# Kernel tuning notes

Hardware: AMD Instinct MI355X
Metric: run time of the kernel (lower is better)

## Reference

```python
import jax, jax.numpy as jnp
import numpy as np

N = 10000   # nodes
E = 160000  # edges (avg degree 16)
D_IN = 768
D_HID = 128
HEADS = 4
NEG_SLOPE = 0.2  # PyG GATConv default leaky_relu slope


def setup_inputs() -> dict:
    key = jax.random.key(0)
    ks = jax.random.split(key, 20)
    nrm = lambda k, s, sc: jax.random.normal(k, s, dtype=jnp.float32) * sc
    return {
        "x": nrm(ks[0], (N, D_IN), 1.0),
        "edge_index": jax.random.randint(ks[1], (2, E), 0, N, dtype=jnp.int32),
        "g": nrm(ks[2], (N, D_IN), 1.0),
        # project: Linear(768,128)
        "proj_W": nrm(ks[3], (D_IN, D_HID), D_IN ** -0.5),
        "proj_b": nrm(ks[4], (D_HID,), 0.01),
        # gat1: GATConv(128,128,heads=4), concat -> 512
        "gat1_W": nrm(ks[5], (D_HID, HEADS * D_HID), D_HID ** -0.5),
        "gat1_att_src": nrm(ks[6], (HEADS, D_HID), D_HID ** -0.5),
        "gat1_att_dst": nrm(ks[7], (HEADS, D_HID), D_HID ** -0.5),
        "gat1_bias": nrm(ks[8], (HEADS * D_HID,), 0.01),
        # gat2: GATConv(512,128), heads=1
        "gat2_W": nrm(ks[9], (HEADS * D_HID, D_HID), (HEADS * D_HID) ** -0.5),
        "gat2_att_src": nrm(ks[10], (1, D_HID), D_HID ** -0.5),
        "gat2_att_dst": nrm(ks[11], (1, D_HID), D_HID ** -0.5),
        "gat2_bias": nrm(ks[12], (D_HID,), 0.01),
        # decoder: Linear(128,768)
        "dec_W": nrm(ks[13], (D_HID, D_IN), D_HID ** -0.5),
        "dec_b": nrm(ks[14], (D_IN,), 0.01),
        "beta": jnp.asarray(0.1, dtype=jnp.float32),
    }


def _leaky_relu(x):
    return jnp.where(x > 0, x, NEG_SLOPE * x)


def _gat_conv(x, W, att_src, att_dst, bias, src, dst, n_nodes, heads, out_ch, concat):
    # x: [N, F_in]; edge (src -> dst), aggregation at dst (PyG convention)
    h = (x @ W).reshape(n_nodes, heads, out_ch)            # [N, H, C]
    a_src = jnp.sum(h * att_src, axis=-1)                  # [N, H]
    a_dst = jnp.sum(h * att_dst, axis=-1)                  # [N, H]
    e = _leaky_relu(a_src[src] + a_dst[dst])               # [E, H]
    # segment softmax over incoming edges of each dst node (numerically stable)
    m = jax.lax.stop_gradient(jax.ops.segment_max(e, dst, num_segments=n_nodes))
    ex = jnp.exp(e - m[dst])
    s = jax.ops.segment_sum(ex, dst, num_segments=n_nodes)
    alpha = ex / (s[dst] + 1e-16)                          # [E, H]
    msg = h[src] * alpha[:, :, None]                       # [E, H, C] gather + weight
    out = jax.ops.segment_sum(msg, dst, num_segments=n_nodes)  # scatter-add -> [N, H, C]
    out = out.reshape(n_nodes, heads * out_ch) if concat else out[:, 0, :]
    return out + bias


def reference(x, edge_index, g, proj_W, proj_b,
              gat1_W, gat1_att_src, gat1_att_dst, gat1_bias,
              gat2_W, gat2_att_src, gat2_att_dst, gat2_bias,
              dec_W, dec_b, beta):
    n = x.shape[0]
    # PyG GATConv default add_self_loops=True
    loop = jnp.arange(n, dtype=edge_index.dtype)
    src = jnp.concatenate([edge_index[0], loop])
    dst = jnp.concatenate([edge_index[1], loop])

    xp = x @ proj_W + proj_b                               # [N, 128]
    h = _gat_conv(xp, gat1_W, gat1_att_src, gat1_att_dst, gat1_bias,
                  src, dst, n, HEADS, D_HID, concat=True)  # [N, 512]
    h = jax.nn.elu(h)
    h = _gat_conv(h, gat2_W, gat2_att_src, gat2_att_dst, gat2_bias,
                  src, dst, n, 1, D_HID, concat=False)     # [N, 128]
    gp = g @ proj_W + proj_b                               # [N, 128]
    h = h + beta * gp
    return h @ dec_W + dec_b                               # [N, 768]
```

## Files before the change

### kernel.cpp

```cpp
#include <hip/hip_runtime.h>
#include <math.h>

#define N_NODES 10000
#define N_EDGES 160000
#define ET      (N_EDGES + N_NODES)
#define NRG     313
#define AZS     ((size_t)NRG * 4096)

typedef unsigned short u16;
typedef __attribute__((ext_vector_type(8))) short bf16x8;
typedef __attribute__((ext_vector_type(4))) float f32x4;

__device__ __forceinline__ u16 f2bf(float f) {
    union { float f; unsigned u; } v; v.f = f;
    unsigned r = (v.u + 0x7FFFu + ((v.u >> 16) & 1u)) >> 16;
    return (u16)r;
}
__device__ __forceinline__ float bf2f(u16 b) {
    union { unsigned u; float f; } v; v.u = ((unsigned)b) << 16;
    return v.f;
}

__device__ __forceinline__ void split1(float f, u16& h, u16& l) {
    unsigned u = __float_as_uint(f);
    h = (u16)(u >> 16);
    l = f2bf(f - __uint_as_float(u & 0xffff0000u));
}

__device__ __forceinline__ void splitA8(const float* __restrict__ p,
                                        bf16x8& hv, bf16x8& lv) {
    float4 v0 = *reinterpret_cast<const float4*>(p);
    float4 v1 = *reinterpret_cast<const float4*>(p + 4);
    float f[8] = {v0.x, v0.y, v0.z, v0.w, v1.x, v1.y, v1.z, v1.w};
    bf16x8 h, l;
#pragma unroll
    for (int i = 0; i < 8; ++i) {
        unsigned u = __float_as_uint(f[i]);
        h[i] = (short)(u >> 16);
        float r = f[i] - __uint_as_float(u & 0xffff0000u);
        l[i] = (short)(__float_as_uint(r) >> 16);
    }
    hv = h; lv = l;
}

__device__ __forceinline__ size_t packA_off(int row, int k) {
    int rg = row >> 5, fm = (row >> 4) & 1, lr = row & 15;
    int kb = k >> 5, q = (k >> 3) & 3, j = k & 7;
    return ((((size_t)rg * 4 + kb) * 2 + fm) * 64 + q * 16 + lr) * 8 + j;
}

#define MFMA3(A_h, A_l, B_h, B_l, ACC)                                            \
    ACC = __builtin_amdgcn_mfma_f32_16x16x32_bf16(A_h, B_h, ACC, 0, 0, 0);        \
    ACC = __builtin_amdgcn_mfma_f32_16x16x32_bf16(A_h, B_l, ACC, 0, 0, 0);        \
    ACC = __builtin_amdgcn_mfma_f32_16x16x32_bf16(A_l, B_h, ACC, 0, 0, 0);

#define GLD16(SRC, DST)                                                           \
    __builtin_amdgcn_global_load_lds(                                             \
        (const __attribute__((address_space(1))) void*)(SRC),                     \
        (__attribute__((address_space(3))) void*)(DST), 16, 0, 0)

__global__ void prep_kernel(const float* __restrict__ W0, u16* p0h, u16* p0l,
                            const float* __restrict__ W1, u16* p1h, u16* p1l,
                            const float* __restrict__ W2, u16* p2h, u16* p2l,
                            const float* __restrict__ W3, u16* p3h, u16* p3l,
                            const float* __restrict__ att_src,
                            const float* __restrict__ att_dst,
                            float* __restrict__ vas, float* __restrict__ vad,
                            int* __restrict__ deg) {
    int b = blockIdx.x, tid = threadIdx.x;
    if (b < 160) {
        int idx = b * 256 + tid;
        const float* W; u16 *oh, *ol; int K, N, rel;
        if      (idx < 12288) { W = W0; oh = p0h; ol = p0l; K = 768; N = 128; rel = idx; }
        else if (idx < 20480) { W = W1; oh = p1h; ol = p1l; K = 128; N = 512; rel = idx - 12288; }
        else if (idx < 28672) { W = W2; oh = p2h; ol = p2l; K = 512; N = 128; rel = idx - 20480; }
        else                  { W = W3; oh = p3h; ol = p3l; K = 128; N = 768; rel = idx - 28672; }
        int perCg = (K / 32) * 128;
        int cg = rel / perCg, r2 = rel - cg * perCg;
        int kb = r2 >> 7, r3 = r2 & 127;
        int fn = r3 >> 6, lane = r3 & 63;
        int col = cg * 32 + fn * 16 + (lane & 15);
        int k0  = kb * 32 + (lane >> 4) * 8;
        bf16x8 hv, lv;
#pragma unroll
        for (int j = 0; j < 8; ++j) {
            float v = W[(size_t)(k0 + j) * N + col];
            u16 h = f2bf(v);
            hv[j] = (short)h;
            lv[j] = (short)f2bf(v - bf2f(h));
        }
        *(bf16x8*)(oh + (size_t)rel * 8) = hv;
        *(bf16x8*)(ol + (size_t)rel * 8) = lv;
    } else if (b == 160) {
        for (int it = tid; it < 512; it += 256) {
            int k = it >> 2, h = it & 3;
            float s = 0.0f, d = 0.0f;
            const float* wr = W1 + (size_t)k * 512 + h * 128;
            const float* as = att_src + h * 128;
            const float* ad = att_dst + h * 128;
            for (int c = 0; c < 128; ++c) {
                float w = wr[c];
                s = fmaf(w, as[c], s);
                d = fmaf(w, ad[c], d);
            }
            vas[k * 4 + h] = s;
            vad[k * 4 + h] = d;
        }
    } else {
        int i = (b - 161) * 256 + tid;
        if (i < N_NODES) deg[i] = 0;
    }
}

template<int K, int SRCSEL, int ZC, int ACT, int LDOUT>
__global__ __launch_bounds__(256)
void mmT_kernel(const float* __restrict__ A0, const float* __restrict__ A1,
                size_t azs,
                const u16* __restrict__ Bh, const u16* __restrict__ Bl,
                const float* __restrict__ bias,
                float* __restrict__ out0, float* __restrict__ out1) {
    constexpr int NS = K / 64;
    __shared__ float smem[2 * 2080];
    const int lane = threadIdx.x & 63;
    const int wid  = threadIdx.x >> 6;
    const int lr = lane & 15, q = lane >> 4;
    const int row0 = blockIdx.x * 32;
    const int z = blockIdx.z;
    const int gcb = blockIdx.y * 128 + z * ZC;

    const float* Ab = SRCSEL ? (z ? A1 : A0) : (A0 + (size_t)z * azs);
    float* outp = (SRCSEL && z) ? out1 : out0;

    const int srow = min(row0 + (lane >> 1), N_NODES - 1);
    const float* sA = Ab + (size_t)srow * K + (lane & 1) * 4;
    float* dg0 = smem + (wid * 2 + 0) * 260;
    float* dg1 = smem + (wid * 2 + 1) * 260;

    const int cg = gcb / 32 + wid;
    const u16* pbh = Bh + (size_t)cg * K * 32 + lane * 8;
    const u16* pbl = Bl + (size_t)cg * K * 32 + lane * 8;

    f32x4 acc[2][2];
#pragma unroll
    for (int i = 0; i < 2; ++i)
#pragma unroll
        for (int j = 0; j < 2; ++j) acc[i][j] = (f32x4){0.f, 0.f, 0.f, 0.f};

    bf16x8 rbh[2][2][2], rbl[2][2][2];

#define STAGE_T(BUF, S) do {                                                   \
        GLD16(sA + (S) * 64 + (wid * 2 + 0) * 8, dg0 + (BUF) * 2080);          \
        GLD16(sA + (S) * 64 + (wid * 2 + 1) * 8, dg1 + (BUF) * 2080);          \
    } while (0)

    STAGE_T(0, 0);
#pragma unroll
    for (int fn = 0; fn < 2; ++fn)
#pragma unroll
        for (int ks = 0; ks < 2; ++ks) {
            rbh[0][fn][ks] = *(const bf16x8*)(pbh + (ks * 2 + fn) * 512);
            rbl[0][fn][ks] = *(const bf16x8*)(pbl + (ks * 2 + fn) * 512);
        }
    __syncthreads();

#pragma unroll
    for (int s = 0; s < NS; ++s) {
        const int bank = s & 1;
        if (s + 1 < NS) {
            STAGE_T(bank ^ 1, s + 1);
#pragma unroll
            for (int fn = 0; fn < 2; ++fn)
#pragma unroll
                for (int ks = 0; ks < 2; ++ks) {
                    rbh[bank ^ 1][fn][ks] =
                        *(const bf16x8*)(pbh + (((s + 1) * 2 + ks) * 2 + fn) * 512);
                    rbl[bank ^ 1][fn][ks] =
                        *(const bf16x8*)(pbl + (((s + 1) * 2 + ks) * 2 + fn) * 512);
                }
        }
        const float* lb = smem + bank * 2080;
        bf16x8 ah[2][2], al[2][2];
#pragma unroll
        for (int fm = 0; fm < 2; ++fm)
#pragma unroll
            for (int ks = 0; ks < 2; ++ks) {
                const float* fp = lb + (ks * 4 + q) * 260 + (fm * 16 + lr) * 8;
                splitA8(fp, ah[fm][ks], al[fm][ks]);
            }
#pragma unroll
        for (int fm = 0; fm < 2; ++fm)
#pragma unroll
            for (int fn = 0; fn < 2; ++fn)
#pragma unroll
                for (int ks = 0; ks < 2; ++ks) {
                    MFMA3(ah[fm][ks], al[fm][ks],
                          rbh[bank][fn][ks], rbl[bank][fn][ks], acc[fm][fn]);
                }
        __syncthreads();
    }

    int orq = q * 4;
#pragma unroll
    for (int fm = 0; fm < 2; ++fm)
#pragma unroll
        for (int fn = 0; fn < 2; ++fn) {
            int col = gcb + wid * 32 + fn * 16 + lr;
            float bb = bias ? bias[col] : 0.0f;
#pragma unroll
            for (int i = 0; i < 4; ++i) {
                int orow = row0 + fm * 16 + orq + i;
                if (orow < N_NODES) {
                    float r = acc[fm][fn][i] + bb;
                    if (ACT == 1) r = r > 0.0f ? r : expm1f(r);
                    outp[(size_t)orow * LDOUT + col] = r;
                }
            }
        }
#undef STAGE_T
}

template<int ZC, int ACT, int LDOUT>
__global__ __launch_bounds__(256)
void mmP_kernel(const u16* __restrict__ Ah, const u16* __restrict__ Al,
                size_t azs,
                const u16* __restrict__ Bh, const u16* __restrict__ Bl,
                const float* __restrict__ bias,
                float* __restrict__ out) {
    constexpr int K = 128;
    const int lane = threadIdx.x & 63;
    const int wid  = threadIdx.x >> 6;
    const int lr = lane & 15, q = lane >> 4;
    const int rg = blockIdx.x;
    const int row0 = rg * 32;
    const int z = blockIdx.z;
    const int gcb = blockIdx.y * 128 + z * ZC;

    const u16* ah = Ah + (size_t)z * azs + (size_t)rg * 4096 + lane * 8;
    const u16* al = Al + (size_t)z * azs + (size_t)rg * 4096 + lane * 8;
    const int cg = gcb / 32 + wid;
    const u16* bh = Bh + (size_t)cg * K * 32 + lane * 8;
    const u16* bl = Bl + (size_t)cg * K * 32 + lane * 8;

    f32x4 acc[2][2];
#pragma unroll
    for (int i = 0; i < 2; ++i)
#pragma unroll
        for (int j = 0; j < 2; ++j) acc[i][j] = (f32x4){0.f, 0.f, 0.f, 0.f};

#pragma unroll
    for (int kb = 0; kb < 4; ++kb) {
        bf16x8 a0h = *(const bf16x8*)(ah + (kb * 2 + 0) * 512);
        bf16x8 a1h = *(const bf16x8*)(ah + (kb * 2 + 1) * 512);
        bf16x8 a0l = *(const bf16x8*)(al + (kb * 2 + 0) * 512);
        bf16x8 a1l = *(const bf16x8*)(al + (kb * 2 + 1) * 512);
        bf16x8 b0h = *(const bf16x8*)(bh + (kb * 2 + 0) * 512);
        bf16x8 b1h = *(const bf16x8*)(bh + (kb * 2 + 1) * 512);
        bf16x8 b0l = *(const bf16x8*)(bl + (kb * 2 + 0) * 512);
        bf16x8 b1l = *(const bf16x8*)(bl + (kb * 2 + 1) * 512);
        MFMA3(a0h, a0l, b0h, b0l, acc[0][0]);
        MFMA3(a0h, a0l, b1h, b1l, acc[0][1]);
        MFMA3(a1h, a1l, b0h, b0l, acc[1][0]);
        MFMA3(a1h, a1l, b1h, b1l, acc[1][1]);
    }

    int orq = q * 4;
#pragma unroll
    for (int fm = 0; fm < 2; ++fm)
#pragma unroll
        for (int fn = 0; fn < 2; ++fn) {
            int col = gcb + wid * 32 + fn * 16 + lr;
            float bb = bias[col];
#pragma unroll
            for (int i = 0; i < 4; ++i) {
                int orow = row0 + fm * 16 + orq + i;
                if (orow < N_NODES) {
                    float r = acc[fm][fn][i] + bb;
                    if (ACT == 1) r = r > 0.0f ? r : expm1f(r);
                    out[(size_t)orow * LDOUT + col] = r;
                }
            }
        }
}

__global__ void att1_kernel(const float* __restrict__ xp,
                            const float* __restrict__ vas,
                            const float* __restrict__ vad,
                            float* __restrict__ as, float* __restrict__ ad) {
    int wv = threadIdx.x >> 6, lane = threadIdx.x & 63;
    int n = blockIdx.x * 4 + wv;
    float2 v = *reinterpret_cast<const float2*>(xp + (size_t)n * 128 + lane * 2);
    float4 s0 = *reinterpret_cast<const float4*>(vas + (lane * 2) * 4);
    float4 s1 = *reinterpret_cast<const float4*>(vas + (lane * 2 + 1) * 4);
    float4 d0 = *reinterpret_cast<const float4*>(vad + (lane * 2) * 4);
    float4 d1 = *reinterpret_cast<const float4*>(vad + (lane * 2 + 1) * 4);
    float ss[4] = { v.x * s0.x + v.y * s1.x, v.x * s0.y + v.y * s1.y,
                    v.x * s0.z + v.y * s1.z, v.x * s0.w + v.y * s1.w };
    float dd[4] = { v.x * d0.x + v.y * d1.x, v.x * d0.y + v.y * d1.y,
                    v.x * d0.z + v.y * d1.z, v.x * d0.w + v.y * d1.w };
#pragma unroll
    for (int m = 32; m > 0; m >>= 1)
#pragma unroll
        for (int h = 0; h < 4; ++h) {
            ss[h] += __shfl_xor(ss[h], m, 64);
            dd[h] += __shfl_xor(dd[h], m, 64);
        }
    if (lane == 0) {
#pragma unroll
        for (int h = 0; h < 4; ++h) {
            as[(size_t)n * 4 + h] = ss[h];
            ad[(size_t)n * 4 + h] = dd[h];
        }
    }
}

__global__ void att2_kernel(const float* __restrict__ h,
                            const float* __restrict__ att_src,
                            const float* __restrict__ att_dst,
                            float* __restrict__ as, float* __restrict__ ad) {
    int wv = threadIdx.x >> 6, lane = threadIdx.x & 63;
    int n = blockIdx.x * 4 + wv;
    const float* hp = h + (size_t)n * 128 + lane * 2;
    float2 v = *reinterpret_cast<const float2*>(hp);
    float2 a = *reinterpret_cast<const float2*>(att_src + lane * 2);
    float2 b = *reinterpret_cast<const float2*>(att_dst + lane * 2);
    float ss = v.x * a.x + v.y * a.y;
    float sd = v.x * b.x + v.y * b.y;
#pragma unroll
    for (int m = 32; m > 0; m >>= 1) {
        ss += __shfl_xor(ss, m, 64);
        sd += __shfl_xor(sd, m, 64);
    }
    if (lane == 0) { as[n] = ss; ad[n] = sd; }
}

__global__ void deg_kernel(const int* __restrict__ ei, int* __restrict__ deg) {
    int e = blockIdx.x * blockDim.x + threadIdx.x;
    if (e >= ET) return;
    int d = (e < N_EDGES) ? ei[N_EDGES + e] : (e - N_EDGES);
    atomicAdd(&deg[d], 1);
}

__global__ void scan1_kernel(const int* __restrict__ deg, int* __restrict__ bsum) {
    __shared__ int sm[256];
    int i = blockIdx.x * 256 + threadIdx.x;
    sm[threadIdx.x] = (i < N_NODES) ? deg[i] : 0;
    __syncthreads();
    for (int s = 128; s > 0; s >>= 1) {
        if (threadIdx.x < s) sm[threadIdx.x] += sm[threadIdx.x + s];
        __syncthreads();
    }
    if (threadIdx.x == 0) bsum[blockIdx.x] = sm[0];
}

__global__ void scan3_kernel(const int* __restrict__ deg, const int* __restrict__ bsum,
                             int* __restrict__ off, int* __restrict__ cur) {
    __shared__ int sm[256];
    __shared__ int sb[40];
    __shared__ int bofs;
    int tid = threadIdx.x;
    if (tid < 40) sb[tid] = bsum[tid];
    int i = blockIdx.x * 256 + tid;
    int v = (i < N_NODES) ? deg[i] : 0;
    sm[tid] = v;
    __syncthreads();
    if (tid == 0) {
        int s = 0;
        for (int b = 0; b < blockIdx.x; ++b) s += sb[b];
        bofs = s;
    }
    for (int s = 1; s < 256; s <<= 1) {
        int t = (tid >= s) ? sm[tid - s] : 0;
        __syncthreads();
        sm[tid] += t;
        __syncthreads();
    }
    if (i < N_NODES) {
        int ex = bofs + sm[tid] - v;
        off[i] = ex;
        cur[i] = ex;
    }
    if (blockIdx.x == 0 && tid == 0) off[N_NODES] = ET;
}

__global__ void fill_kernel(const int* __restrict__ ei,
                            int* __restrict__ cur, int* __restrict__ csr_src) {
    int e = blockIdx.x * blockDim.x + threadIdx.x;
    if (e >= ET) return;
    int s, d;
    if (e < N_EDGES) { s = ei[e]; d = ei[N_EDGES + e]; }
    else             { s = e - N_EDGES; d = s; }
    int pos = atomicAdd(&cur[d], 1);
    csr_src[pos] = s;
}

__global__ __launch_bounds__(128)
void smagg1_kernel(const float* __restrict__ xp,
                   const float* __restrict__ a1s, const float* __restrict__ a1d,
                   const int* __restrict__ off, const int* __restrict__ csr,
                   u16* __restrict__ aggPh, u16* __restrict__ aggPl) {
    int n = blockIdx.x;
    int tid = threadIdx.x, lane = tid & 63, wv = tid >> 6;
    int o0 = off[n], o1 = off[n + 1];
    __shared__ float red[2][8];
    __shared__ float wsh[128][4];
    __shared__ int   ssh[128];

    float4 adv = *reinterpret_cast<const float4*>(a1d + (size_t)n * 4);
    float adn[4] = {adv.x, adv.y, adv.z, adv.w};

    float m[4] = {-1e30f, -1e30f, -1e30f, -1e30f};
    for (int j = o0 + tid; j < o1; j += 128) {
        int sn = csr[j];
        float4 asv = *reinterpret_cast<const float4*>(a1s + (size_t)sn * 4);
        float e0 = asv.x + adn[0]; e0 = e0 > 0.f ? e0 : 0.2f * e0; m[0] = fmaxf(m[0], e0);
        float e1 = asv.y + adn[1]; e1 = e1 > 0.f ? e1 : 0.2f * e1; m[1] = fmaxf(m[1], e1);
        float e2 = asv.z + adn[2]; e2 = e2 > 0.f ? e2 : 0.2f * e2; m[2] = fmaxf(m[2], e2);
        float e3 = asv.w + adn[3]; e3 = e3 > 0.f ? e3 : 0.2f * e3; m[3] = fmaxf(m[3], e3);
    }
#pragma unroll
    for (int mk = 32; mk > 0; mk >>= 1)
#pragma unroll
        for (int h = 0; h < 4; ++h) m[h] = fmaxf(m[h], __shfl_xor(m[h], mk, 64));
    if (lane == 0)
#pragma unroll
        for (int h = 0; h < 4; ++h) red[wv][h] = m[h];
    __syncthreads();
#pragma unroll
    for (int h = 0; h < 4; ++h) m[h] = fmaxf(red[0][h], red[1][h]);

    float s4[4] = {0.f, 0.f, 0.f, 0.f};
    for (int j = o0 + tid; j < o1; j += 128) {
        int sn = csr[j];
        float4 asv = *reinterpret_cast<const float4*>(a1s + (size_t)sn * 4);
        float e0 = asv.x + adn[0]; e0 = e0 > 0.f ? e0 : 0.2f * e0; s4[0] += expf(e0 - m[0]);
        float e1 = asv.y + adn[1]; e1 = e1 > 0.f ? e1 : 0.2f * e1; s4[1] += expf(e1 - m[1]);
        float e2 = asv.z + adn[2]; e2 = e2 > 0.f ? e2 : 0.2f * e2; s4[2] += expf(e2 - m[2]);
        float e3 = asv.w + adn[3]; e3 = e3 > 0.f ? e3 : 0.2f * e3; s4[3] += expf(e3 - m[3]);
    }
#pragma unroll
    for (int mk = 32; mk > 0; mk >>= 1)
#pragma unroll
        for (int h = 0; h < 4; ++h) s4[h] += __shfl_xor(s4[h], mk, 64);
    if (lane == 0)
#pragma unroll
        for (int h = 0; h < 4; ++h) red[wv][4 + h] = s4[h];
    __syncthreads();
    float inv[4];
#pragma unroll
    for (int h = 0; h < 4; ++h) inv[h] = 1.0f / (red[0][4 + h] + red[1][4 + h] + 1e-16f);

    float a0 = 0.f, a1 = 0.f, a2 = 0.f, a3 = 0.f;
    for (int base = o0; base < o1; base += 128) {
        __syncthreads();
        int j = base + tid;
        if (j < o1) {
            int sn = csr[j];
            ssh[tid] = sn;
            float4 asv = *reinterpret_cast<const float4*>(a1s + (size_t)sn * 4);
            float e0 = asv.x + adn[0]; e0 = e0 > 0.f ? e0 : 0.2f * e0; wsh[tid][0] = expf(e0 - m[0]);
            float e1 = asv.y + adn[1]; e1 = e1 > 0.f ? e1 : 0.2f * e1; wsh[tid][1] = expf(e1 - m[1]);
            float e2 = asv.z + adn[2]; e2 = e2 > 0.f ? e2 : 0.2f * e2; wsh[tid][2] = expf(e2 - m[2]);
            float e3 = asv.w + adn[3]; e3 = e3 > 0.f ? e3 : 0.2f * e3; wsh[tid][3] = expf(e3 - m[3]);
        }
        __syncthreads();
        int cnt = min(128, o1 - base);
        for (int e2i = 0; e2i < cnt; ++e2i) {
            float v = xp[(size_t)ssh[e2i] * 128 + tid];
            float4 w = *reinterpret_cast<const float4*>(&wsh[e2i][0]);
            a0 = fmaf(w.x, v, a0); a1 = fmaf(w.y, v, a1);
            a2 = fmaf(w.z, v, a2); a3 = fmaf(w.w, v, a3);
        }
    }

    float r[4] = {a0 * inv[0], a1 * inv[1], a2 * inv[2], a3 * inv[3]};
    size_t po = packA_off(n, tid);
#pragma unroll
    for (int h = 0; h < 4; ++h) {
        u16 hi, lo;
        split1(r[h], hi, lo);
        aggPh[(size_t)h * AZS + po] = hi;
        aggPl[(size_t)h * AZS + po] = lo;
    }
}

__global__ __launch_bounds__(128)
void smgather2_kernel(const float* __restrict__ h2,
                      const float* __restrict__ a2s, const float* __restrict__ a2d,
                      const int* __restrict__ off, const int* __restrict__ csr,
                      const float* __restrict__ bias,
                      u16* __restrict__ outPh, u16* __restrict__ outPl,
                      const float* __restrict__ gp,
                      const float* __restrict__ beta_p) {
    int n = blockIdx.x;
    int tid = threadIdx.x, lane = tid & 63, wv = tid >> 6;
    int o0 = off[n], o1 = off[n + 1];
    __shared__ float red[2][2];
    __shared__ float wsh[128];
    __shared__ int   ssh[128];

    float adn = a2d[n];
    float m = -1e30f;
    for (int j = o0 + tid; j < o1; j += 128) {
        float e = a2s[csr[j]] + adn;
        e = e > 0.f ? e : 0.2f * e;
        m = fmaxf(m, e);
    }
#pragma unroll
    for (int mk = 32; mk > 0; mk >>= 1) m = fmaxf(m, __shfl_xor(m, mk, 64));
    if (lane == 0) red[wv][0] = m;
    __syncthreads();
    m = fmaxf(red[0][0], red[1][0]);

    float s = 0.f;
    for (int j = o0 + tid; j < o1; j += 128) {
        float e = a2s[csr[j]] + adn;
        e = e > 0.f ? e : 0.2f * e;
        s += expf(e - m);
    }
#pragma unroll
    for (int mk = 32; mk > 0; mk >>= 1) s += __shfl_xor(s, mk, 64);
    if (lane == 0) red[wv][1] = s;
    __syncthreads();
    float inv = 1.0f / (red[0][1] + red[1][1] + 1e-16f);

    float acc = 0.f;
    for (int base = o0; base < o1; base += 128) {
        __syncthreads();
        int j = base + tid;
        if (j < o1) {
            int sn = csr[j];
            ssh[tid] = sn;
            float e = a2s[sn] + adn;
            e = e > 0.f ? e : 0.2f * e;
            wsh[tid] = expf(e - m);
        }
        __syncthreads();
        int cnt = min(128, o1 - base);
        for (int e2i = 0; e2i < cnt; ++e2i) {
            acc = fmaf(wsh[e2i], h2[(size_t)ssh[e2i] * 128 + tid], acc);
        }
    }

    float r = acc * inv + bias[tid] + beta_p[0] * gp[(size_t)n * 128 + tid];
    u16 hi, lo;
    split1(r, hi, lo);
    size_t po = packA_off(n, tid);
    outPh[po] = hi;
    outPl[po] = lo;
}

extern "C" void kernel_launch(void* const* d_in, const int* in_sizes, int n_in,
                              void* d_out, int out_size, void* d_ws, size_t ws_size,
                              hipStream_t stream) {
    const float* x      = (const float*)d_in[0];
    const int*   ei     = (const int*)  d_in[1];
    const float* g      = (const float*)d_in[2];
    const float* proj_W = (const float*)d_in[3];
    const float* proj_b = (const float*)d_in[4];
    const float* gat1_W = (const float*)d_in[5];
    const float* g1_as  = (const float*)d_in[6];
    const float* g1_ad  = (const float*)d_in[7];
    const float* gat1_b = (const float*)d_in[8];
    const float* gat2_W = (const float*)d_in[9];
    const float* g2_as  = (const float*)d_in[10];
    const float* g2_ad  = (const float*)d_in[11];
    const float* gat2_b = (const float*)d_in[12];
    const float* dec_W  = (const float*)d_in[13];
    const float* dec_b  = (const float*)d_in[14];
    const float* beta   = (const float*)d_in[15];
    float* out = (float*)d_out;

    char* p = (char*)d_ws;
    auto alloc = [&](size_t b) { void* r = (void*)p; p += (b + 255) & ~(size_t)255; return r; };
    float* helu  = (float*)alloc((size_t)10000 * 512 * 4);
    u16*   aggPh = (u16*)alloc(4 * AZS * 2);
    u16*   aggPl = (u16*)alloc(4 * AZS * 2);
    u16*   hfPh  = (u16*)alloc(AZS * 2);
    u16*   hfPl  = (u16*)alloc(AZS * 2);
    float* xp    = (float*)alloc((size_t)10000 * 128 * 4);
    float* gp    = (float*)alloc((size_t)10000 * 128 * 4);
    u16*   pwh   = (u16*)alloc(768 * 128 * 2);
    u16*   pwl   = (u16*)alloc(768 * 128 * 2);
    u16*   w1h   = (u16*)alloc(128 * 512 * 2);
    u16*   w1l   = (u16*)alloc(128 * 512 * 2);
    u16*   w2h   = (u16*)alloc(512 * 128 * 2);
    u16*   w2l   = (u16*)alloc(512 * 128 * 2);
    u16*   wdh   = (u16*)alloc(128 * 768 * 2);
    u16*   wdl   = (u16*)alloc(128 * 768 * 2);
    float* va1s  = (float*)alloc(128 * 4 * 4);
    float* va1d  = (float*)alloc(128 * 4 * 4);
    float* a1s   = (float*)alloc((size_t)N_NODES * 4 * 4);
    float* a1d   = (float*)alloc((size_t)N_NODES * 4 * 4);
    float* a2s   = (float*)alloc((size_t)N_NODES * 4);
    float* a2d   = (float*)alloc((size_t)N_NODES * 4);
    int*   deg   = (int*)alloc((size_t)N_NODES * 4);
    int*   off   = (int*)alloc((size_t)(N_NODES + 1) * 4);
    int*   cur   = (int*)alloc((size_t)N_NODES * 4);
    int*   csr   = (int*)alloc((size_t)ET * 4);
    int*   bsum  = (int*)alloc(64 * 4);
    float* h2 = xp;

    hipLaunchKernelGGL(prep_kernel, dim3(201), dim3(256), 0, stream,
                       proj_W, pwh, pwl, gat1_W, w1h, w1l,
                       gat2_W, w2h, w2l, dec_W, wdh, wdl,
                       g1_as, g1_ad, va1s, va1d, deg);
    hipLaunchKernelGGL(deg_kernel, dim3((ET + 255) / 256), dim3(256), 0, stream, ei, deg);
    hipLaunchKernelGGL(scan1_kernel, dim3(40), dim3(256), 0, stream, deg, bsum);
    hipLaunchKernelGGL(scan3_kernel, dim3(40), dim3(256), 0, stream, deg, bsum, off, cur);
    hipLaunchKernelGGL(fill_kernel, dim3((ET + 255) / 256), dim3(256), 0, stream, ei, cur, csr);

    hipLaunchKernelGGL((mmT_kernel<768, 1, 0, 0, 128>), dim3(NRG, 1, 2), dim3(256), 0, stream,
                       x, g, (size_t)0, pwh, pwl, proj_b, xp, gp);

    hipLaunchKernelGGL(att1_kernel, dim3(N_NODES / 4), dim3(256), 0, stream,
                       xp, va1s, va1d, a1s, a1d);
    hipLaunchKernelGGL(smagg1_kernel, dim3(N_NODES), dim3(128), 0, stream,
                       xp, a1s, a1d, off, csr, aggPh, aggPl);
    hipLaunchKernelGGL((mmP_kernel<128, 1, 512>), dim3(NRG, 1, 4), dim3(256), 0, stream,
                       aggPh, aggPl, AZS, w1h, w1l, gat1_b, helu);

    hipLaunchKernelGGL((mmT_kernel<512, 0, 0, 0, 128>), dim3(NRG, 1, 1), dim3(256), 0, stream,
                       helu, (const float*)nullptr, (size_t)0,
                       w2h, w2l, (const float*)nullptr, h2, (float*)nullptr);
    hipLaunchKernelGGL(att2_kernel, dim3(N_NODES / 4), dim3(256), 0, stream,
                       h2, g2_as, g2_ad, a2s, a2d);
    hipLaunchKernelGGL(smgather2_kernel, dim3(N_NODES), dim3(128), 0, stream,
                       h2, a2s, a2d, off, csr, gat2_b, hfPh, hfPl, gp, beta);

    hipLaunchKernelGGL((mmP_kernel<0, 0, 768>), dim3(NRG, 6, 1), dim3(256), 0, stream,
                       hfPh, hfPl, (size_t)0, wdh, wdl, dec_b, out);
}
```

Before: 180.0 us.

## Replace LDS-staged fp32-A GEMM with register-direct 16-row tile kernel

```diff
diff --git a/kernel.cpp b/kernel.cpp
--- a/kernel.cpp
+++ b/kernel.cpp
@@ -27,10 +27,8 @@
     l = f2bf(f - __uint_as_float(u & 0xffff0000u));
 }
 
-__device__ __forceinline__ void splitA8(const float* __restrict__ p,
-                                        bf16x8& hv, bf16x8& lv) {
-    float4 v0 = *reinterpret_cast<const float4*>(p);
-    float4 v1 = *reinterpret_cast<const float4*>(p + 4);
+__device__ __forceinline__ void splitR(const float4& v0, const float4& v1,
+                                       bf16x8& hv, bf16x8& lv) {
     float f[8] = {v0.x, v0.y, v0.z, v0.w, v1.x, v1.y, v1.z, v1.w};
     bf16x8 h, l;
 #pragma unroll
@@ -53,11 +51,6 @@
     ACC = __builtin_amdgcn_mfma_f32_16x16x32_bf16(A_h, B_h, ACC, 0, 0, 0);        \
     ACC = __builtin_amdgcn_mfma_f32_16x16x32_bf16(A_h, B_l, ACC, 0, 0, 0);        \
     ACC = __builtin_amdgcn_mfma_f32_16x16x32_bf16(A_l, B_h, ACC, 0, 0, 0);
-
-#define GLD16(SRC, DST)                                                           \
-    __builtin_amdgcn_global_load_lds(                                             \
-        (const __attribute__((address_space(1))) void*)(SRC),                     \
-        (__attribute__((address_space(3))) void*)(DST), 16, 0, 0)
 
 __global__ void prep_kernel(const float* __restrict__ W0, u16* p0h, u16* p0l,
                             const float* __restrict__ W1, u16* p1h, u16* p1l,
@@ -112,111 +105,73 @@
     }
 }
 
-template<int K, int SRCSEL, int ZC, int ACT, int LDOUT>
+template<int K, int SRCSEL, int ACT, int LDOUT>
 __global__ __launch_bounds__(256)
-void mmT_kernel(const float* __restrict__ A0, const float* __restrict__ A1,
-                size_t azs,
-                const u16* __restrict__ Bh, const u16* __restrict__ Bl,
-                const float* __restrict__ bias,
-                float* __restrict__ out0, float* __restrict__ out1) {
-    constexpr int NS = K / 64;
-    __shared__ float smem[2 * 2080];
+void mmRP_kernel(const float* __restrict__ A0, const float* __restrict__ A1,
+                 const u16* __restrict__ Bh, const u16* __restrict__ Bl,
+                 const float* __restrict__ bias,
+                 float* __restrict__ out0, float* __restrict__ out1) {
+    constexpr int NS = K / 32;
     const int lane = threadIdx.x & 63;
     const int wid  = threadIdx.x >> 6;
     const int lr = lane & 15, q = lane >> 4;
-    const int row0 = blockIdx.x * 32;
+    const int row0 = blockIdx.x * 16;
     const int z = blockIdx.z;
-    const int gcb = blockIdx.y * 128 + z * ZC;
-
-    const float* Ab = SRCSEL ? (z ? A1 : A0) : (A0 + (size_t)z * azs);
+    const int gcb = blockIdx.y * 128 + wid * 32;
+
+    const float* Ab = SRCSEL ? (z ? A1 : A0) : A0;
     float* outp = (SRCSEL && z) ? out1 : out0;
 
-    const int srow = min(row0 + (lane >> 1), N_NODES - 1);
-    const float* sA = Ab + (size_t)srow * K + (lane & 1) * 4;
-    float* dg0 = smem + (wid * 2 + 0) * 260;
-    float* dg1 = smem + (wid * 2 + 1) * 260;
-
-    const int cg = gcb / 32 + wid;
+    const float* pa = Ab + (size_t)(row0 + lr) * K + q * 8;
+    const int cg = gcb / 32;
     const u16* pbh = Bh + (size_t)cg * K * 32 + lane * 8;
     const u16* pbl = Bl + (size_t)cg * K * 32 + lane * 8;
 
-    f32x4 acc[2][2];
-#pragma unroll
-    for (int i = 0; i < 2; ++i)
-#pragma unroll
-        for (int j = 0; j < 2; ++j) acc[i][j] = (f32x4){0.f, 0.f, 0.f, 0.f};
-
-    bf16x8 rbh[2][2][2], rbl[2][2][2];
-
-#define STAGE_T(BUF, S) do {                                                   \
-        GLD16(sA + (S) * 64 + (wid * 2 + 0) * 8, dg0 + (BUF) * 2080);          \
-        GLD16(sA + (S) * 64 + (wid * 2 + 1) * 8, dg1 + (BUF) * 2080);          \
-    } while (0)
-
-    STAGE_T(0, 0);
-#pragma unroll
-    for (int fn = 0; fn < 2; ++fn)
-#pragma unroll
-        for (int ks = 0; ks < 2; ++ks) {
-            rbh[0][fn][ks] = *(const bf16x8*)(pbh + (ks * 2 + fn) * 512);
-            rbl[0][fn][ks] = *(const bf16x8*)(pbl + (ks * 2 + fn) * 512);
-        }
-    __syncthreads();
-
-#pragma unroll
-    for (int s = 0; s < NS; ++s) {
-        const int bank = s & 1;
-        if (s + 1 < NS) {
-            STAGE_T(bank ^ 1, s + 1);
-#pragma unroll
-            for (int fn = 0; fn < 2; ++fn)
-#pragma unroll
-                for (int ks = 0; ks < 2; ++ks) {
-                    rbh[bank ^ 1][fn][ks] =
-                        *(const bf16x8*)(pbh + (((s + 1) * 2 + ks) * 2 + fn) * 512);
-                    rbl[bank ^ 1][fn][ks] =
-                        *(const bf16x8*)(pbl + (((s + 1) * 2 + ks) * 2 + fn) * 512);
-                }
-        }
-        const float* lb = smem + bank * 2080;
-        bf16x8 ah[2][2], al[2][2];
-#pragma unroll
-        for (int fm = 0; fm < 2; ++fm)
-#pragma unroll
-            for (int ks = 0; ks < 2; ++ks) {
-                const float* fp = lb + (ks * 4 + q) * 260 + (fm * 16 + lr) * 8;
-                splitA8(fp, ah[fm][ks], al[fm][ks]);
-            }
-#pragma unroll
-        for (int fm = 0; fm < 2; ++fm)
-#pragma unroll
-            for (int fn = 0; fn < 2; ++fn)
-#pragma unroll
-                for (int ks = 0; ks < 2; ++ks) {
-                    MFMA3(ah[fm][ks], al[fm][ks],
-                          rbh[bank][fn][ks], rbl[bank][fn][ks], acc[fm][fn]);
-                }
-        __syncthreads();
-    }
-
-    int orq = q * 4;
-#pragma unroll
-    for (int fm = 0; fm < 2; ++fm)
-#pragma unroll
-        for (int fn = 0; fn < 2; ++fn) {
-            int col = gcb + wid * 32 + fn * 16 + lr;
-            float bb = bias ? bias[col] : 0.0f;
-#pragma unroll
-            for (int i = 0; i < 4; ++i) {
-                int orow = row0 + fm * 16 + orq + i;
-                if (orow < N_NODES) {
-                    float r = acc[fm][fn][i] + bb;
-                    if (ACT == 1) r = r > 0.0f ? r : expm1f(r);
-                    outp[(size_t)orow * LDOUT + col] = r;
-                }
-            }
-        }
-#undef STAGE_T
+    f32x4 acc0 = (f32x4){0.f, 0.f, 0.f, 0.f};
+    f32x4 acc1 = (f32x4){0.f, 0.f, 0.f, 0.f};
+
+    float4 aLo[2], aHi[2];
+    bf16x8 rb0h[2], rb1h[2], rb0l[2], rb1l[2];
+
+    aLo[0]  = *(const float4*)(pa);
+    aHi[0]  = *(const float4*)(pa + 4);
+    rb0h[0] = *(const bf16x8*)(pbh + 0 * 512);
+    rb1h[0] = *(const bf16x8*)(pbh + 1 * 512);
+    rb0l[0] = *(const bf16x8*)(pbl + 0 * 512);
+    rb1l[0] = *(const bf16x8*)(pbl + 1 * 512);
+
+#pragma unroll
+    for (int kb = 0; kb < NS; ++kb) {
+        const int cur = kb & 1, nxt = cur ^ 1;
+        if (kb + 1 < NS) {
+            aLo[nxt]  = *(const float4*)(pa + (kb + 1) * 32);
+            aHi[nxt]  = *(const float4*)(pa + (kb + 1) * 32 + 4);
+            rb0h[nxt] = *(const bf16x8*)(pbh + ((kb + 1) * 2 + 0) * 512);
+            rb1h[nxt] = *(const bf16x8*)(pbh + ((kb + 1) * 2 + 1) * 512);
+            rb0l[nxt] = *(const bf16x8*)(pbl + ((kb + 1) * 2 + 0) * 512);
+            rb1l[nxt] = *(const bf16x8*)(pbl + ((kb + 1) * 2 + 1) * 512);
+        }
+        bf16x8 ah, al;
+        splitR(aLo[cur], aHi[cur], ah, al);
+        MFMA3(ah, al, rb0h[cur], rb0l[cur], acc0);
+        MFMA3(ah, al, rb1h[cur], rb1l[cur], acc1);
+    }
+
+    int c0 = gcb + lr, c1 = gcb + 16 + lr;
+    float bb0 = bias ? bias[c0] : 0.0f;
+    float bb1 = bias ? bias[c1] : 0.0f;
+#pragma unroll
+    for (int i = 0; i < 4; ++i) {
+        int orow = row0 + q * 4 + i;
+        float r0 = acc0[i] + bb0;
+        float r1 = acc1[i] + bb1;
+        if (ACT == 1) {
+            r0 = r0 > 0.0f ? r0 : expm1f(r0);
+            r1 = r1 > 0.0f ? r1 : expm1f(r1);
+        }
+        outp[(size_t)orow * LDOUT + c0] = r0;
+        outp[(size_t)orow * LDOUT + c1] = r1;
+    }
 }
 
 template<int ZC, int ACT, int LDOUT>
@@ -609,8 +564,8 @@
     hipLaunchKernelGGL(scan3_kernel, dim3(40), dim3(256), 0, stream, deg, bsum, off, cur);
     hipLaunchKernelGGL(fill_kernel, dim3((ET + 255) / 256), dim3(256), 0, stream, ei, cur, csr);
 
-    hipLaunchKernelGGL((mmT_kernel<768, 1, 0, 0, 128>), dim3(NRG, 1, 2), dim3(256), 0, stream,
-                       x, g, (size_t)0, pwh, pwl, proj_b, xp, gp);
+    hipLaunchKernelGGL((mmRP_kernel<768, 1, 0, 128>), dim3(625, 1, 2), dim3(256), 0, stream,
+                       x, g, pwh, pwl, proj_b, xp, gp);
 
     hipLaunchKernelGGL(att1_kernel, dim3(N_NODES / 4), dim3(256), 0, stream,
                        xp, va1s, va1d, a1s, a1d);
@@ -619,9 +574,9 @@
     hipLaunchKernelGGL((mmP_kernel<128, 1, 512>), dim3(NRG, 1, 4), dim3(256), 0, stream,
                        aggPh, aggPl, AZS, w1h, w1l, gat1_b, helu);
 
-    hipLaunchKernelGGL((mmT_kernel<512, 0, 0, 0, 128>), dim3(NRG, 1, 1), dim3(256), 0, stream,
-                       helu, (const float*)nullptr, (size_t)0,
-                       w2h, w2l, (const float*)nullptr, h2, (float*)nullptr);
+    hipLaunchKernelGGL((mmRP_kernel<512, 0, 0, 128>), dim3(625, 1, 1), dim3(256), 0, stream,
+                       helu, (const float*)nullptr, w2h, w2l,
+                       (const float*)nullptr, h2, (float*)nullptr);
     hipLaunchKernelGGL(att2_kernel, dim3(N_NODES / 4), dim3(256), 0, stream,
                        h2, g2_as, g2_ad, a2s, a2d);
     hipLaunchKernelGGL(smgather2_kernel, dim3(N_NODES), dim3(128), 0, stream,
```

After: 208.0 us. 15.5% more time.

## Split-K the projection and GAT2 GEMMs with separate reduction kernels

Applied to the files above, without the earlier changes.

```diff
diff --git a/kernel.cpp b/kernel.cpp
--- a/kernel.cpp
+++ b/kernel.cpp
@@ -6,6 +6,7 @@
 #define ET      (N_EDGES + N_NODES)
 #define NRG     313
 #define AZS     ((size_t)NRG * 4096)
+#define PSLOT   1280000
 
 typedef unsigned short u16;
 typedef __attribute__((ext_vector_type(8))) short bf16x8;
@@ -112,33 +113,30 @@
     }
 }
 
-template<int K, int SRCSEL, int ZC, int ACT, int LDOUT>
+template<int KTOT, int SK, int SRCSEL>
 __global__ __launch_bounds__(256)
-void mmT_kernel(const float* __restrict__ A0, const float* __restrict__ A1,
-                size_t azs,
-                const u16* __restrict__ Bh, const u16* __restrict__ Bl,
-                const float* __restrict__ bias,
-                float* __restrict__ out0, float* __restrict__ out1) {
-    constexpr int NS = K / 64;
+void mmTS_kernel(const float* __restrict__ A0, const float* __restrict__ A1,
+                 const u16* __restrict__ Bh, const u16* __restrict__ Bl,
+                 float* __restrict__ pp) {
+    constexpr int KS = KTOT / SK;
+    constexpr int NS = KS / 64;
     __shared__ float smem[2 * 2080];
     const int lane = threadIdx.x & 63;
     const int wid  = threadIdx.x >> 6;
     const int lr = lane & 15, q = lane >> 4;
     const int row0 = blockIdx.x * 32;
     const int z = blockIdx.z;
-    const int gcb = blockIdx.y * 128 + z * ZC;
-
-    const float* Ab = SRCSEL ? (z ? A1 : A0) : (A0 + (size_t)z * azs);
-    float* outp = (SRCSEL && z) ? out1 : out0;
+    const int k0 = blockIdx.y * KS;
+
+    const float* Ab = SRCSEL ? (z ? A1 : A0) : A0;
 
     const int srow = min(row0 + (lane >> 1), N_NODES - 1);
-    const float* sA = Ab + (size_t)srow * K + (lane & 1) * 4;
+    const float* sA = Ab + (size_t)srow * KTOT + (lane & 1) * 4 + k0;
     float* dg0 = smem + (wid * 2 + 0) * 260;
     float* dg1 = smem + (wid * 2 + 1) * 260;
 
-    const int cg = gcb / 32 + wid;
-    const u16* pbh = Bh + (size_t)cg * K * 32 + lane * 8;
-    const u16* pbl = Bl + (size_t)cg * K * 32 + lane * 8;
+    const u16* pbh = Bh + (size_t)wid * KTOT * 32 + (size_t)k0 * 32 + lane * 8;
+    const u16* pbl = Bl + (size_t)wid * KTOT * 32 + (size_t)k0 * 32 + lane * 8;
 
     f32x4 acc[2][2];
 #pragma unroll
@@ -199,24 +197,48 @@
         __syncthreads();
     }
 
+    float* pbase = pp + (size_t)(z * SK + blockIdx.y) * PSLOT;
     int orq = q * 4;
 #pragma unroll
     for (int fm = 0; fm < 2; ++fm)
 #pragma unroll
         for (int fn = 0; fn < 2; ++fn) {
-            int col = gcb + wid * 32 + fn * 16 + lr;
-            float bb = bias ? bias[col] : 0.0f;
+            int col = wid * 32 + fn * 16 + lr;
 #pragma unroll
             for (int i = 0; i < 4; ++i) {
                 int orow = row0 + fm * 16 + orq + i;
-                if (orow < N_NODES) {
-                    float r = acc[fm][fn][i] + bb;
-                    if (ACT == 1) r = r > 0.0f ? r : expm1f(r);
-                    outp[(size_t)orow * LDOUT + col] = r;
-                }
+                if (orow < N_NODES)
+                    pbase[(size_t)orow * 128 + col] = acc[fm][fn][i];
             }
         }
 #undef STAGE_T
+}
+
+__global__ void proj_reduce_kernel(const float* __restrict__ pp,
+                                   const float* __restrict__ bias,
+                                   float* __restrict__ xp, float* __restrict__ gp) {
+    int i = blockIdx.x * blockDim.x + threadIdx.x;
+    if (i >= 2 * 320000) return;
+    int src = i / 320000;
+    int r = i - src * 320000;
+    const float4* p4 = reinterpret_cast<const float4*>(pp);
+    float4 a = p4[(size_t)(src * 2 + 0) * 320000 + r];
+    float4 b = p4[(size_t)(src * 2 + 1) * 320000 + r];
+    float4 bb = reinterpret_cast<const float4*>(bias)[r & 31];
+    float4 o = make_float4(a.x + b.x + bb.x, a.y + b.y + bb.y,
+                           a.z + b.z + bb.z, a.w + b.w + bb.w);
+    reinterpret_cast<float4*>(src ? gp : xp)[r] = o;
+}
+
+__global__ void gat2_reduce_kernel(const float* __restrict__ pp,
+                                   float* __restrict__ h2) {
+    int r = blockIdx.x * blockDim.x + threadIdx.x;
+    if (r >= 320000) return;
+    const float4* p4 = reinterpret_cast<const float4*>(pp);
+    float4 a = p4[r], b = p4[320000 + r], c = p4[640000 + r], d = p4[960000 + r];
+    reinterpret_cast<float4*>(h2)[r] =
+        make_float4(a.x + b.x + c.x + d.x, a.y + b.y + c.y + d.y,
+                    a.z + b.z + c.z + d.z, a.w + b.w + c.w + d.w);
 }
 
 template<int ZC, int ACT, int LDOUT>
@@ -598,7 +620,9 @@
     int*   cur   = (int*)alloc((size_t)N_NODES * 4);
     int*   csr   = (int*)alloc((size_t)ET * 4);
     int*   bsum  = (int*)alloc(64 * 4);
-    float* h2 = xp;
+    float* h2      = xp;
+    float* pp_proj = helu;
+    float* pp_g2   = (float*)aggPh;
 
     hipLaunchKernelGGL(prep_kernel, dim3(201), dim3(256), 0, stream,
                        proj_W, pwh, pwl, gat1_W, w1h, w1l,
@@ -609,8 +633,10 @@
     hipLaunchKernelGGL(scan3_kernel, dim3(40), dim3(256), 0, stream, deg, bsum, off, cur);
     hipLaunchKernelGGL(fill_kernel, dim3((ET + 255) / 256), dim3(256), 0, stream, ei, cur, csr);
 
-    hipLaunchKernelGGL((mmT_kernel<768, 1, 0, 0, 128>), dim3(NRG, 1, 2), dim3(256), 0, stream,
-                       x, g, (size_t)0, pwh, pwl, proj_b, xp, gp);
+    hipLaunchKernelGGL((mmTS_kernel<768, 2, 1>), dim3(NRG, 2, 2), dim3(256), 0, stream,
+                       x, g, pwh, pwl, pp_proj);
+    hipLaunchKernelGGL(proj_reduce_kernel, dim3(2500), dim3(256), 0, stream,
+                       pp_proj, proj_b, xp, gp);
 
     hipLaunchKernelGGL(att1_kernel, dim3(N_NODES / 4), dim3(256), 0, stream,
                        xp, va1s, va1d, a1s, a1d);
@@ -619,9 +645,10 @@
     hipLaunchKernelGGL((mmP_kernel<128, 1, 512>), dim3(NRG, 1, 4), dim3(256), 0, stream,
                        aggPh, aggPl, AZS, w1h, w1l, gat1_b, helu);
 
-    hipLaunchKernelGGL((mmT_kernel<512, 0, 0, 0, 128>), dim3(NRG, 1, 1), dim3(256), 0, stream,
-                       helu, (const float*)nullptr, (size_t)0,
-                       w2h, w2l, (const float*)nullptr, h2, (float*)nullptr);
+    hipLaunchKernelGGL((mmTS_kernel<512, 4, 0>), dim3(NRG, 4, 1), dim3(256), 0, stream,
+                       helu, (const float*)nullptr, w2h, w2l, pp_g2);
+    hipLaunchKernelGGL(gat2_reduce_kernel, dim3(1250), dim3(256), 0, stream,
+                       pp_g2, h2);
     hipLaunchKernelGGL(att2_kernel, dim3(N_NODES / 4), dim3(256), 0, stream,
                        h2, g2_as, g2_ad, a2s, a2d);
     hipLaunchKernelGGL(smgather2_kernel, dim3(N_NODES), dim3(128), 0, stream,
```

New measurement: 189.0 us. 5.0% more time.
